# Kernel tuning notes

Measured on AMD Instinct MI355X. Metric: run time of the kernel, lower is better.

## Reference

```python
import jax, jax.numpy as jnp
import numpy as np

B, S, D = 4, 2048, 1024

def setup_inputs() -> dict:
    key = jax.random.key(0)
    k1, k2, k3, k4 = jax.random.split(key, 4)
    scale = 1.0 / np.sqrt(D)
    token_encodings = jax.random.normal(k1, (B, S, D), dtype=jnp.float32)
    W_q = jax.random.normal(k2, (D, D), dtype=jnp.float32) * scale
    W_k = jax.random.normal(k3, (D, D), dtype=jnp.float32) * scale
    W_v = jax.random.normal(k4, (D, D), dtype=jnp.float32) * scale
    # causal mask, broadcastable to (B, S, S); 0 means masked
    mask = jnp.tril(jnp.ones((S, S), dtype=jnp.int32))[None, :, :]
    return {"token_encodings": token_encodings, "mask": mask,
            "W_q": W_q, "W_k": W_k, "W_v": W_v}

def reference(token_encodings, mask, W_q, W_k, W_v):
    # nn.Linear(d, d, bias=False): y = x @ W.T
    q = jnp.einsum('bsd,ed->bse', token_encodings, W_q)
    k = jnp.einsum('bsd,ed->bse', token_encodings, W_k)
    v = jnp.einsum('bsd,ed->bse', token_encodings, W_v)
    d_k = q.shape[-1]
    scores = jnp.einsum('bqd,bkd->bqk', q, k) / jnp.sqrt(jnp.asarray(d_k, q.dtype))
    scores = jnp.where(mask == 0, jnp.asarray(-jnp.inf, scores.dtype), scores)
    attn_weights = jax.nn.softmax(scores, axis=-1)
    output = jnp.einsum('bqk,bkd->bqd', attn_weights, v)
    return (output, attn_weights)
```

## Files before the change

kernel.cpp:

```cpp
#include <hip/hip_runtime.h>
#include <hip/hip_bf16.h>
#include <stdint.h>
#include <math.h>


typedef __hip_bfloat16 bf16;
typedef __attribute__((ext_vector_type(8))) short short8;
typedef __attribute__((ext_vector_type(4))) float f32x4;

#define BM 128
#define BN 128
#define BK 64

static constexpr int Bb = 4;
static constexpr int S  = 2048;
static constexpr int D  = 1024;
static constexpr size_t QK_ELEMS = (size_t)Bb * S * D;
static constexpr size_t SS_ELEMS = (size_t)S * S;
static constexpr size_t W_ELEMS  = (size_t)D * D;

__device__ __forceinline__ void async16(const bf16* g, bf16* l) {
  __builtin_amdgcn_global_load_lds(
      (__attribute__((address_space(1))) const void*)g,
      (__attribute__((address_space(3))) void*)l, 16, 0, 0);
}

template<bool SWAP>
__device__ __forceinline__ void gemm_core(const bf16* __restrict__ A,
                                          const bf16* __restrict__ B,
                                          int ldA, int ldB, int ksteps,
                                          bf16* As, bf16* Bs,
                                          f32x4 acc[4][4])
{
  const int tid  = threadIdx.x;
  const int lane = tid & 63;
  const int wave = tid >> 6;
  const int wm   = (wave & 1) * 64;
  const int wn   = (wave >> 1) * 64;
  const int m16  = lane & 15;
  const int kq   = lane >> 4;
  const int sw   = m16 & 7;

  int r[4], f[4];
  #pragma unroll
  for (int i = 0; i < 4; ++i) {
    const int c = tid + i * 256;
    r[i] = c >> 3;
    f[i] = (((c & 7) ^ (r[i] & 7))) * 8;
  }

  for (int ks = 0; ks < ksteps; ++ks) {
    const int k = ks * BK;
    #pragma unroll
    for (int i = 0; i < 4; ++i)
      async16(A + (size_t)r[i] * ldA + k + f[i], As + ((size_t)tid + i * 256) * 8);
    #pragma unroll
    for (int i = 0; i < 4; ++i)
      async16(B + (size_t)r[i] * ldB + k + f[i], Bs + ((size_t)tid + i * 256) * 8);
    __syncthreads();

    #pragma unroll
    for (int j = 0; j < 2; ++j) {
      const int jc = j * 4 + kq;
      const int sl = jc ^ sw;
      short8 af[4], bfr[4];
      #pragma unroll
      for (int i = 0; i < 4; ++i)
        af[i] = *(const short8*)&As[((wm + i * 16 + m16) * 8 + sl) * 8];
      #pragma unroll
      for (int i = 0; i < 4; ++i)
        bfr[i] = *(const short8*)&Bs[((wn + i * 16 + m16) * 8 + sl) * 8];

      #pragma unroll
      for (int mi = 0; mi < 4; ++mi) {
        #pragma unroll
        for (int ni = 0; ni < 4; ++ni) {
          if (SWAP)
            acc[mi][ni] = __builtin_amdgcn_mfma_f32_16x16x32_bf16(
                bfr[ni], af[mi], acc[mi][ni], 0, 0, 0);
          else
            acc[mi][ni] = __builtin_amdgcn_mfma_f32_16x16x32_bf16(
                af[mi], bfr[ni], acc[mi][ni], 0, 0, 0);
        }
      }
    }
    __syncthreads();
  }
}

__device__ __forceinline__ void zero_acc(f32x4 acc[4][4]) {
  #pragma unroll
  for (int mi = 0; mi < 4; ++mi)
    #pragma unroll
    for (int ni = 0; ni < 4; ++ni)
      acc[mi][ni] = (f32x4){0.f, 0.f, 0.f, 0.f};
}

__device__ __forceinline__ void gemm_core64(const bf16* __restrict__ A,
                                            const bf16* __restrict__ B,
                                            int ldA, int ldB, int ksteps,
                                            bf16* As, bf16* Bs,
                                            f32x4 acc[4][2])
{
  const int tid  = threadIdx.x;
  const int lane = tid & 63;
  const int wave = tid >> 6;
  const int wn   = wave * 32;
  const int m16  = lane & 15;
  const int kq   = lane >> 4;
  const int sw   = m16 & 7;

  int ra[2], fa[2], rb[4], fb[4];
  #pragma unroll
  for (int i = 0; i < 2; ++i) {
    const int c = tid + i * 256;
    ra[i] = c >> 3;
    fa[i] = ((c & 7) ^ (ra[i] & 7)) * 8;
  }
  #pragma unroll
  for (int i = 0; i < 4; ++i) {
    const int c = tid + i * 256;
    rb[i] = c >> 3;
    fb[i] = ((c & 7) ^ (rb[i] & 7)) * 8;
  }

  for (int ks = 0; ks < ksteps; ++ks) {
    const int k = ks * BK;
    #pragma unroll
    for (int i = 0; i < 2; ++i)
      async16(A + (size_t)ra[i] * ldA + k + fa[i], As + ((size_t)tid + i * 256) * 8);
    #pragma unroll
    for (int i = 0; i < 4; ++i)
      async16(B + (size_t)rb[i] * ldB + k + fb[i], Bs + ((size_t)tid + i * 256) * 8);
    __syncthreads();

    #pragma unroll
    for (int j = 0; j < 2; ++j) {
      const int jc = j * 4 + kq;
      const int sl = jc ^ sw;
      short8 af[4], bfr[2];
      #pragma unroll
      for (int i = 0; i < 4; ++i)
        af[i] = *(const short8*)&As[((i * 16 + m16) * 8 + sl) * 8];
      #pragma unroll
      for (int i = 0; i < 2; ++i)
        bfr[i] = *(const short8*)&Bs[((wn + i * 16 + m16) * 8 + sl) * 8];

      #pragma unroll
      for (int mi = 0; mi < 4; ++mi)
        #pragma unroll
        for (int ni = 0; ni < 2; ++ni)
          acc[mi][ni] = __builtin_amdgcn_mfma_f32_16x16x32_bf16(
              af[mi], bfr[ni], acc[mi][ni], 0, 0, 0);
    }
    __syncthreads();
  }
}

__device__ __forceinline__ void zero_acc64(f32x4 acc[4][2]) {
  #pragma unroll
  for (int mi = 0; mi < 4; ++mi)
    #pragma unroll
    for (int ni = 0; ni < 2; ++ni)
      acc[mi][ni] = (f32x4){0.f, 0.f, 0.f, 0.f};
}

__device__ __forceinline__ unsigned short f2b(float f) {
  __hip_bfloat16 h = __float2bfloat16(f);
  return *(unsigned short*)&h;
}

__global__ __launch_bounds__(256)
void cvt_kernel(const float* __restrict__ X,  const float* __restrict__ Wq,
                const float* __restrict__ Wk, const float* __restrict__ Wv,
                bf16* __restrict__ Xb, bf16* __restrict__ Wqb,
                bf16* __restrict__ Wkb, bf16* __restrict__ Wvb)
{
  const size_t g = ((size_t)blockIdx.x * 256 + threadIdx.x) * 4;
  const float* src; bf16* dst; size_t off;
  if (g < QK_ELEMS) { src = X; dst = Xb; off = g; }
  else {
    const size_t h = g - QK_ELEMS;
    const int w = (int)(h >> 20);
    off = h & (W_ELEMS - 1);
    src = (w == 0) ? Wq : (w == 1) ? Wk : Wv;
    dst = (w == 0) ? Wqb : (w == 1) ? Wkb : Wvb;
  }
  const float4 v = *(const float4*)(src + off);
  uint2 o;
  o.x = (uint32_t)f2b(v.x) | ((uint32_t)f2b(v.y) << 16);
  o.y = (uint32_t)f2b(v.z) | ((uint32_t)f2b(v.w) << 16);
  *(uint2*)((unsigned short*)dst + off) = o;
}

__global__ __launch_bounds__(256, 4)
void qkv_kernel(const bf16* __restrict__ X, const bf16* __restrict__ Wq,
                const bf16* __restrict__ Wk, const bf16* __restrict__ Wv,
                bf16* __restrict__ Q, bf16* __restrict__ Ko,
                bf16* __restrict__ Vt)
{
  __shared__ __align__(16) bf16 As[BM * BK];
  __shared__ __align__(16) bf16 Bs[BN * BK];
  const int L = blockIdx.x;
  const int x = L & 7;
  const int s = L >> 3;
  const int nt  = s & 7;
  const int zmt = ((s >> 3) << 3) | x;
  const int z   = zmt >> 6;
  const int mt  = zmt & 63;
  const bf16* W = (z == 0) ? Wq : (z == 1) ? Wk : Wv;

  const int lane = threadIdx.x & 63, wave = threadIdx.x >> 6;
  const int wm = (wave & 1) * 64, wn = (wave >> 1) * 64;
  const int col0 = lane & 15, row0 = (lane >> 4) * 4;

  f32x4 acc[4][4];
  zero_acc(acc);
  if (z < 2) {
    gemm_core<false>(X + (size_t)mt * 128 * D, W + (size_t)nt * 128 * D,
                     D, D, D / BK, As, Bs, acc);
    bf16* Out = z ? Ko : Q;
    #pragma unroll
    for (int mi = 0; mi < 4; ++mi)
      #pragma unroll
      for (int ni = 0; ni < 4; ++ni)
        #pragma unroll
        for (int r = 0; r < 4; ++r) {
          const int grow = mt * 128 + wm + mi * 16 + row0 + r;
          const int gcol = nt * 128 + wn + ni * 16 + col0;
          Out[(size_t)grow * D + gcol] = __float2bfloat16(acc[mi][ni][r]);
        }
  } else {
    gemm_core<true>(X + (size_t)mt * 128 * D, W + (size_t)nt * 128 * D,
                    D, D, D / BK, As, Bs, acc);
    const int b = (mt * 128) >> 11;
    #pragma unroll
    for (int mi = 0; mi < 4; ++mi)
      #pragma unroll
      for (int ni = 0; ni < 4; ++ni)
        #pragma unroll
        for (int r = 0; r < 4; ++r) {
          const int ge = nt * 128 + wn + ni * 16 + row0 + r;
          const int gs = mt * 128 + wm + mi * 16 + col0;
          const int sl = gs & (S - 1);
          Vt[(size_t)b * D * S + (size_t)ge * S + sl] = __float2bfloat16(acc[mi][ni][r]);
        }
  }
}

__global__ __launch_bounds__(256, 4)
void scores_kernel(const bf16* __restrict__ Q, const bf16* __restrict__ K,
                   float* __restrict__ Sc)
{
  const int t = blockIdx.x, b = blockIdx.y;
  int m = (int)((sqrtf(4.f * (float)t + 1.f) - 1.f) * 0.5f);
  while ((m + 1) * (m + 2) <= t) ++m;
  while (m * (m + 1) > t) --m;
  const int r_ = t - m * (m + 1);
  const int qi = 2 * m + (r_ > m ? 1 : 0);
  const int kt = (r_ > m) ? (r_ - (m + 1)) : r_;

  __shared__ __align__(16) bf16 As[64 * BK];
  __shared__ __align__(16) bf16 Bs[128 * BK];

  f32x4 acc[4][2];
  zero_acc64(acc);
  gemm_core64(Q + ((size_t)b * S + qi * 64) * D,
              K + ((size_t)b * S + kt * 128) * D,
              D, D, D / BK, As, Bs, acc);

  const int lane = threadIdx.x & 63, wave = threadIdx.x >> 6;
  const int col0 = lane & 15, row0 = (lane >> 4) * 4;
  float* out = Sc + (size_t)b * SS_ELEMS;
  #pragma unroll
  for (int mi = 0; mi < 4; ++mi)
    #pragma unroll
    for (int ni = 0; ni < 2; ++ni)
      #pragma unroll
      for (int r = 0; r < 4; ++r) {
        const int gq = qi * 64 + mi * 16 + row0 + r;
        const int gk = kt * 128 + wave * 32 + ni * 16 + col0;
        out[(size_t)gq * S + gk] = acc[mi][ni][r] * 0.03125f;
      }
}

__device__ __forceinline__ float wave_max(float v) {
  #pragma unroll
  for (int o = 32; o > 0; o >>= 1) v = fmaxf(v, __shfl_xor(v, o, 64));
  return v;
}
__device__ __forceinline__ float wave_sum(float v) {
  #pragma unroll
  for (int o = 32; o > 0; o >>= 1) v += __shfl_xor(v, o, 64);
  return v;
}

__global__ __launch_bounds__(256)
void softmax_kernel(float* __restrict__ Attn, bf16* __restrict__ Pb)
{
  const int row = blockIdx.x;
  const int b = row >> 11, i = row & (S - 1);
  float* s = Attn + (size_t)b * SS_ELEMS + (size_t)i * S;
  bf16* p  = Pb   + (size_t)b * SS_ELEMS + (size_t)i * S;
  const int t = threadIdx.x;
  const int lane = t & 63, wave = t >> 6;
  __shared__ float red[4];

  float4 v[2];
  #pragma unroll
  for (int u = 0; u < 2; ++u) {
    const int base = (t + u * 256) * 4;
    if (base + 3 <= i) {
      v[u] = *(const float4*)(s + base);
    } else if (base > i) {
      v[u] = make_float4(-INFINITY, -INFINITY, -INFINITY, -INFINITY);
    } else {
      v[u].x = (base + 0 <= i) ? s[base + 0] : -INFINITY;
      v[u].y = (base + 1 <= i) ? s[base + 1] : -INFINITY;
      v[u].z = (base + 2 <= i) ? s[base + 2] : -INFINITY;
      v[u].w = (base + 3 <= i) ? s[base + 3] : -INFINITY;
    }
  }

  float m = -INFINITY;
  #pragma unroll
  for (int u = 0; u < 2; ++u)
    m = fmaxf(m, fmaxf(fmaxf(v[u].x, v[u].y), fmaxf(v[u].z, v[u].w)));
  m = wave_max(m);
  if (lane == 0) red[wave] = m;
  __syncthreads();
  m = fmaxf(fmaxf(red[0], red[1]), fmaxf(red[2], red[3]));
  __syncthreads();

  float sum = 0.f;
  #pragma unroll
  for (int u = 0; u < 2; ++u) {
    v[u].x = __expf(v[u].x - m); sum += v[u].x;
    v[u].y = __expf(v[u].y - m); sum += v[u].y;
    v[u].z = __expf(v[u].z - m); sum += v[u].z;
    v[u].w = __expf(v[u].w - m); sum += v[u].w;
  }
  sum = wave_sum(sum);
  if (lane == 0) red[wave] = sum;
  __syncthreads();
  sum = red[0] + red[1] + red[2] + red[3];
  const float inv = 1.f / sum;

  const int dt_end = ((i >> 7) + 1) * 128;
  #pragma unroll
  for (int u = 0; u < 2; ++u) {
    const int base = (t + u * 256) * 4;
    float4 w;
    w.x = v[u].x * inv; w.y = v[u].y * inv;
    w.z = v[u].z * inv; w.w = v[u].w * inv;
    *(float4*)(s + base) = w;
    if (base < dt_end) {
      ushort4 pk;
      pk.x = f2b(w.x); pk.y = f2b(w.y); pk.z = f2b(w.z); pk.w = f2b(w.w);
      *(ushort4*)((unsigned short*)p + base) = pk;
    }
  }
}

__global__ __launch_bounds__(256, 4)
void out_kernel(const bf16* __restrict__ P, const bf16* __restrict__ Vt,
                float* __restrict__ O)
{
  const int L = blockIdx.x;
  const int x = L & 7;
  const int s = L >> 3;
  const int dt  = s & 7;
  const int qb  = ((s >> 3) << 3) | x;
  const int Qi  = 31 - (qb >> 2);
  const int b   = qb & 3;

  __shared__ __align__(16) bf16 As[64 * BK];
  __shared__ __align__(16) bf16 Bs[128 * BK];

  f32x4 acc[4][2];
  zero_acc64(acc);
  gemm_core64(P + (size_t)b * SS_ELEMS + (size_t)Qi * 64 * S,
              Vt + (size_t)b * D * S + (size_t)dt * 128 * S,
              S, S, Qi + 1, As, Bs, acc);

  const int lane = threadIdx.x & 63, wave = threadIdx.x >> 6;
  const int col0 = lane & 15, row0 = (lane >> 4) * 4;
  #pragma unroll
  for (int mi = 0; mi < 4; ++mi)
    #pragma unroll
    for (int ni = 0; ni < 2; ++ni)
      #pragma unroll
      for (int r = 0; r < 4; ++r) {
        const int gq = Qi * 64 + mi * 16 + row0 + r;
        const int gd = dt * 128 + wave * 32 + ni * 16 + col0;
        O[((size_t)b * S + gq) * D + gd] = acc[mi][ni][r];
      }
}

extern "C" void kernel_launch(void* const* d_in, const int* in_sizes, int n_in,
                              void* d_out, int out_size, void* d_ws, size_t ws_size,
                              hipStream_t stream) {
  const float* X  = (const float*)d_in[0];
  const float* Wq = (const float*)d_in[2];
  const float* Wk = (const float*)d_in[3];
  const float* Wv = (const float*)d_in[4];

  float* Out  = (float*)d_out;
  float* Attn = Out + QK_ELEMS;

  bf16* Q   = (bf16*)d_ws;
  bf16* K   = Q + QK_ELEMS;
  bf16* Vt  = K + QK_ELEMS;
  bf16* Xb  = Vt + QK_ELEMS;
  bf16* Wqb = Xb + QK_ELEMS;
  bf16* Wkb = Wqb + W_ELEMS;
  bf16* Wvb = Wkb + W_ELEMS;
  bf16* Pb  = (bf16*)d_ws;

  const int cvt_blocks = (int)((QK_ELEMS + 3 * W_ELEMS) / 4 / 256);
  cvt_kernel<<<cvt_blocks, 256, 0, stream>>>(X, Wq, Wk, Wv, Xb, Wqb, Wkb, Wvb);
  qkv_kernel<<<dim3(1536), 256, 0, stream>>>(Xb, Wqb, Wkb, Wvb, Q, K, Vt);
  const int ntile64 = 2 * (S / 128) * (S / 128 + 1) / 2;
  scores_kernel<<<dim3(ntile64, Bb), 256, 0, stream>>>(Q, K, Attn);
  softmax_kernel<<<dim3(Bb * S), 256, 0, stream>>>(Attn, Pb);
  out_kernel<<<dim3(1024), 256, 0, stream>>>(Pb, Vt, Out);
}
```

Before: 267.1 us.

## Fold Wq and Wk into a single matrix M = Wq^T Wk to skip the K projection

Rewrites the scores as X Wq^T Wk X^T. A small GEMM first forms M from transposed bf16 copies of Wq and Wk, then computes Y = X M, and the scores kernel multiplies Y by Xb directly. This removes one of the three large projection GEMMs (Q and K become a single Y GEMM) in exchange for a cheap 1024^3 GEMM and a transposing convert. The extra bf16 rounding of M may change accuracy slightly.

After: 274.3 us. 1.03x slower.

```diff
diff --git a/kernel.cpp b/kernel.cpp
--- a/kernel.cpp
+++ b/kernel.cpp
@@ -165,39 +165,90 @@
       acc[mi][ni] = (f32x4){0.f, 0.f, 0.f, 0.f};
 }
 
-__device__ __forceinline__ unsigned short f2b(float f) {
+__device__ __forceinline__ unsigned int f2b(float f) {
   __hip_bfloat16 h = __float2bfloat16(f);
-  return *(unsigned short*)&h;
+  return (unsigned int)*(unsigned short*)&h;
 }
 
 __global__ __launch_bounds__(256)
 void cvt_kernel(const float* __restrict__ X,  const float* __restrict__ Wq,
                 const float* __restrict__ Wk, const float* __restrict__ Wv,
-                bf16* __restrict__ Xb, bf16* __restrict__ Wqb,
-                bf16* __restrict__ Wkb, bf16* __restrict__ Wvb)
-{
-  const size_t g = ((size_t)blockIdx.x * 256 + threadIdx.x) * 4;
-  const float* src; bf16* dst; size_t off;
-  if (g < QK_ELEMS) { src = X; dst = Xb; off = g; }
-  else {
-    const size_t h = g - QK_ELEMS;
-    const int w = (int)(h >> 20);
-    off = h & (W_ELEMS - 1);
-    src = (w == 0) ? Wq : (w == 1) ? Wk : Wv;
-    dst = (w == 0) ? Wqb : (w == 1) ? Wkb : Wvb;
-  }
-  const float4 v = *(const float4*)(src + off);
-  uint2 o;
-  o.x = (uint32_t)f2b(v.x) | ((uint32_t)f2b(v.y) << 16);
-  o.y = (uint32_t)f2b(v.z) | ((uint32_t)f2b(v.w) << 16);
-  *(uint2*)((unsigned short*)dst + off) = o;
+                bf16* __restrict__ Xb, bf16* __restrict__ Wvb,
+                bf16* __restrict__ Wqt, bf16* __restrict__ Wkt)
+{
+  __shared__ unsigned short T[64][72];
+  const int bid = blockIdx.x;
+  const int tid = threadIdx.x;
+  if (bid < 9216) {
+    const size_t g = ((size_t)bid * 256 + tid) * 4;
+    const float* src; bf16* dst; size_t off;
+    if (g < QK_ELEMS) { src = X; dst = Xb; off = g; }
+    else              { src = Wv; dst = Wvb; off = g - QK_ELEMS; }
+    const float4 v = *(const float4*)(src + off);
+    uint2 o;
+    o.x = f2b(v.x) | (f2b(v.y) << 16);
+    o.y = f2b(v.z) | (f2b(v.w) << 16);
+    *(uint2*)((unsigned short*)dst + off) = o;
+  } else {
+    const int tb   = bid - 9216;
+    const int w    = tb >> 8;
+    const int tile = tb & 255;
+    const int ti = tile >> 4, tj = tile & 15;
+    const float* src = w ? Wk : Wq;
+    bf16* dst = w ? Wkt : Wqt;
+    #pragma unroll
+    for (int k = 0; k < 4; ++k) {
+      const int e  = (tid >> 4) + k * 16;
+      const int cg = tid & 15;
+      const float4 v = *(const float4*)(src + (size_t)(tj * 64 + e) * D + ti * 64 + cg * 4);
+      T[cg * 4 + 0][e] = (unsigned short)f2b(v.x);
+      T[cg * 4 + 1][e] = (unsigned short)f2b(v.y);
+      T[cg * 4 + 2][e] = (unsigned short)f2b(v.z);
+      T[cg * 4 + 3][e] = (unsigned short)f2b(v.w);
+    }
+    __syncthreads();
+    #pragma unroll
+    for (int k = 0; k < 2; ++k) {
+      const int i  = (tid >> 3) + k * 32;
+      const int eg = tid & 7;
+      const short8 o = *(const short8*)&T[i][eg * 8];
+      *(short8*)((unsigned short*)dst + (size_t)(ti * 64 + i) * D + tj * 64 + eg * 8) = o;
+    }
+  }
 }
 
 __global__ __launch_bounds__(256, 4)
-void qkv_kernel(const bf16* __restrict__ X, const bf16* __restrict__ Wq,
-                const bf16* __restrict__ Wk, const bf16* __restrict__ Wv,
-                bf16* __restrict__ Q, bf16* __restrict__ Ko,
-                bf16* __restrict__ Vt)
+void mt_kernel(const bf16* __restrict__ Wkt, const bf16* __restrict__ Wqt,
+               bf16* __restrict__ Mt)
+{
+  __shared__ __align__(16) bf16 As[BM * BK];
+  __shared__ __align__(16) bf16 Bs[BN * BK];
+  const int mt = blockIdx.x >> 3, nt = blockIdx.x & 7;
+
+  f32x4 acc[4][4];
+  zero_acc(acc);
+  gemm_core<false>(Wkt + (size_t)mt * 128 * D, Wqt + (size_t)nt * 128 * D,
+                   D, D, D / BK, As, Bs, acc);
+
+  const int lane = threadIdx.x & 63, wave = threadIdx.x >> 6;
+  const int wm = (wave & 1) * 64, wn = (wave >> 1) * 64;
+  const int col0 = lane & 15, row0 = (lane >> 4) * 4;
+  #pragma unroll
+  for (int mi = 0; mi < 4; ++mi)
+    #pragma unroll
+    for (int ni = 0; ni < 4; ++ni)
+      #pragma unroll
+      for (int r = 0; r < 4; ++r) {
+        const int gj = mt * 128 + wm + mi * 16 + row0 + r;
+        const int gi = nt * 128 + wn + ni * 16 + col0;
+        Mt[(size_t)gj * D + gi] = __float2bfloat16(acc[mi][ni][r]);
+      }
+}
+
+__global__ __launch_bounds__(256, 4)
+void yv_kernel(const bf16* __restrict__ Xb, const bf16* __restrict__ Mt,
+               const bf16* __restrict__ Wvb,
+               bf16* __restrict__ Y, bf16* __restrict__ Vt)
 {
   __shared__ __align__(16) bf16 As[BM * BK];
   __shared__ __align__(16) bf16 Bs[BN * BK];
@@ -208,7 +259,6 @@
   const int zmt = ((s >> 3) << 3) | x;
   const int z   = zmt >> 6;
   const int mt  = zmt & 63;
-  const bf16* W = (z == 0) ? Wq : (z == 1) ? Wk : Wv;
 
   const int lane = threadIdx.x & 63, wave = threadIdx.x >> 6;
   const int wm = (wave & 1) * 64, wn = (wave >> 1) * 64;
@@ -216,10 +266,9 @@
 
   f32x4 acc[4][4];
   zero_acc(acc);
-  if (z < 2) {
-    gemm_core<false>(X + (size_t)mt * 128 * D, W + (size_t)nt * 128 * D,
+  if (z == 0) {
+    gemm_core<false>(Xb + (size_t)mt * 128 * D, Mt + (size_t)nt * 128 * D,
                      D, D, D / BK, As, Bs, acc);
-    bf16* Out = z ? Ko : Q;
     #pragma unroll
     for (int mi = 0; mi < 4; ++mi)
       #pragma unroll
@@ -228,10 +277,10 @@
         for (int r = 0; r < 4; ++r) {
           const int grow = mt * 128 + wm + mi * 16 + row0 + r;
           const int gcol = nt * 128 + wn + ni * 16 + col0;
-          Out[(size_t)grow * D + gcol] = __float2bfloat16(acc[mi][ni][r]);
+          Y[(size_t)grow * D + gcol] = __float2bfloat16(acc[mi][ni][r]);
         }
   } else {
-    gemm_core<true>(X + (size_t)mt * 128 * D, W + (size_t)nt * 128 * D,
+    gemm_core<true>(Xb + (size_t)mt * 128 * D, Wvb + (size_t)nt * 128 * D,
                     D, D, D / BK, As, Bs, acc);
     const int b = (mt * 128) >> 11;
     #pragma unroll
@@ -249,7 +298,7 @@
 }
 
 __global__ __launch_bounds__(256, 4)
-void scores_kernel(const bf16* __restrict__ Q, const bf16* __restrict__ K,
+void scores_kernel(const bf16* __restrict__ Y, const bf16* __restrict__ Xb,
                    float* __restrict__ Sc)
 {
   const int t = blockIdx.x, b = blockIdx.y;
@@ -265,8 +314,8 @@
 
   f32x4 acc[4][2];
   zero_acc64(acc);
-  gemm_core64(Q + ((size_t)b * S + qi * 64) * D,
-              K + ((size_t)b * S + kt * 128) * D,
+  gemm_core64(Y + ((size_t)b * S + qi * 64) * D,
+              Xb + ((size_t)b * S + kt * 128) * D,
               D, D, D / BK, As, Bs, acc);
 
   const int lane = threadIdx.x & 63, wave = threadIdx.x >> 6;
@@ -356,7 +405,8 @@
     *(float4*)(s + base) = w;
     if (base < dt_end) {
       ushort4 pk;
-      pk.x = f2b(w.x); pk.y = f2b(w.y); pk.z = f2b(w.z); pk.w = f2b(w.w);
+      pk.x = (unsigned short)f2b(w.x); pk.y = (unsigned short)f2b(w.y);
+      pk.z = (unsigned short)f2b(w.z); pk.w = (unsigned short)f2b(w.w);
       *(ushort4*)((unsigned short*)p + base) = pk;
     }
   }
@@ -408,20 +458,21 @@
   float* Out  = (float*)d_out;
   float* Attn = Out + QK_ELEMS;
 
-  bf16* Q   = (bf16*)d_ws;
-  bf16* K   = Q + QK_ELEMS;
-  bf16* Vt  = K + QK_ELEMS;
-  bf16* Xb  = Vt + QK_ELEMS;
-  bf16* Wqb = Xb + QK_ELEMS;
-  bf16* Wkb = Wqb + W_ELEMS;
-  bf16* Wvb = Wkb + W_ELEMS;
+  bf16* Y   = (bf16*)d_ws;
+  bf16* Xb  = Y + QK_ELEMS;
+  bf16* Vt  = Xb + QK_ELEMS;
+  bf16* Wvb = Vt + QK_ELEMS;
+  bf16* Wqt = Wvb + W_ELEMS;
+  bf16* Wkt = Wqt + W_ELEMS;
+  bf16* Mt  = Wkt + W_ELEMS;
   bf16* Pb  = (bf16*)d_ws;
 
-  const int cvt_blocks = (int)((QK_ELEMS + 3 * W_ELEMS) / 4 / 256);
-  cvt_kernel<<<cvt_blocks, 256, 0, stream>>>(X, Wq, Wk, Wv, Xb, Wqb, Wkb, Wvb);
-  qkv_kernel<<<dim3(1536), 256, 0, stream>>>(Xb, Wqb, Wkb, Wvb, Q, K, Vt);
+  const int cvt_blocks = 9216 + 512;
+  cvt_kernel<<<cvt_blocks, 256, 0, stream>>>(X, Wq, Wk, Wv, Xb, Wvb, Wqt, Wkt);
+  mt_kernel<<<64, 256, 0, stream>>>(Wkt, Wqt, Mt);
+  yv_kernel<<<dim3(1024), 256, 0, stream>>>(Xb, Mt, Wvb, Y, Vt);
   const int ntile64 = 2 * (S / 128) * (S / 128 + 1) / 2;
-  scores_kernel<<<dim3(ntile64, Bb), 256, 0, stream>>>(Q, K, Attn);
+  scores_kernel<<<dim3(ntile64, Bb), 256, 0, stream>>>(Y, Xb, Attn);
   softmax_kernel<<<dim3(Bb * S), 256, 0, stream>>>(Attn, Pb);
   out_kernel<<<dim3(1024), 256, 0, stream>>>(Pb, Vt, Out);
 }
```
